# Kernel optimization log

Measured on AMD Instinct MI355X. Metric: run time of the kernel, lower is better.

Reference implementation:

```python
import jax, jax.numpy as jnp
import numpy as np

N, E, ESM, H_DIM, HEADS, LAYERS = 20000, 640000, 1280, 256, 8, 3
C = H_DIM // HEADS  # per-head channels = 32
B, M = 4096, 8


def setup_inputs() -> dict:
    key = jax.random.key(0)
    ks = jax.random.split(key, 24)
    s = lambda i, *shp: jax.random.normal(ks[i], shp, dtype=jnp.float32) * 0.02
    inp = {
        'x': jax.random.normal(ks[0], (N, ESM), dtype=jnp.float32),
        'edge_index': jax.random.randint(ks[1], (2, E), 0, N),
        'sites': jax.random.randint(ks[2], (B, M), 0, N),
        'mut_onehot': jax.random.normal(ks[3], (B, M, 20), dtype=jnp.float32),
        'mask': jnp.ones((B, M), dtype=bool),
        # params
        'in_W': s(4, ESM, H_DIM), 'in_b': jnp.zeros((H_DIM,), jnp.float32),
        'gat_W': s(5, LAYERS, H_DIM, HEADS * C),
        'att_src': s(6, LAYERS, HEADS, C), 'att_dst': s(7, LAYERS, HEADS, C),
        'gat_b': jnp.zeros((LAYERS, H_DIM), jnp.float32),
        'ln_g': jnp.ones((LAYERS, H_DIM), jnp.float32),
        'ln_b': jnp.zeros((LAYERS, H_DIM), jnp.float32),
        'me_W1': s(8, 20, H_DIM), 'me_b1': jnp.zeros((H_DIM,), jnp.float32),
        'me_W2': s(9, H_DIM, H_DIM), 'me_b2': jnp.zeros((H_DIM,), jnp.float32),
        'pool_q': jax.random.normal(ks[10], (H_DIM,), dtype=jnp.float32),
        'key_W': s(11, H_DIM, H_DIM), 'key_b': jnp.zeros((H_DIM,), jnp.float32),
        'mlp_W1': s(12, H_DIM, H_DIM // 2), 'mlp_b1': jnp.zeros((H_DIM // 2,), jnp.float32),
        'mlp_W2': s(13, H_DIM // 2, 1), 'mlp_b2': jnp.zeros((1,), jnp.float32),
    }
    return inp


def layer_norm(h, g, b, eps=1e-5):
    mu = h.mean(-1, keepdims=True)
    var = ((h - mu) ** 2).mean(-1, keepdims=True)
    return (h - mu) * jax.lax.rsqrt(var + eps) * g + b


def gat_conv(h, src, dst, W, a_src, a_dst, b):
    # PyG GATConv: linear -> per-node attn logits -> edge leaky_relu -> segment softmax over dst -> scatter-sum
    xh = (h @ W).reshape(N, HEADS, C)
    al_s = (xh * a_src).sum(-1)  # [N,H]
    al_d = (xh * a_dst).sum(-1)
    alpha = jax.nn.leaky_relu(al_s[src] + al_d[dst], negative_slope=0.2)  # [E',H]
    mx = jax.ops.segment_max(alpha, dst, num_segments=N)
    ea = jnp.exp(alpha - mx[dst])
    denom = jax.ops.segment_sum(ea, dst, num_segments=N)
    w = ea / (denom[dst] + 1e-16)
    msg = xh[src] * w[:, :, None]  # [E',H,C]
    out = jax.ops.segment_sum(msg, dst, num_segments=N)
    return out.reshape(N, HEADS * C) + b


def reference(x, edge_index, sites, mut_onehot, mask, in_W, in_b, gat_W, att_src, att_dst,
              gat_b, ln_g, ln_b, me_W1, me_b1, me_W2, me_b2, pool_q, key_W, key_b,
              mlp_W1, mlp_b1, mlp_W2, mlp_b2):
    # GATConv default add_self_loops=True
    loops = jnp.arange(N, dtype=edge_index.dtype)
    src = jnp.concatenate([edge_index[0], loops])
    dst = jnp.concatenate([edge_index[1], loops])
    # encode_graph (eval mode: dropout = identity)
    h = x @ in_W + in_b
    for i in range(LAYERS):
        h_new = gat_conv(h, src, dst, gat_W[i], att_src[i][None], att_dst[i][None], gat_b[i])
        h_new = jax.nn.elu(h_new)
        h = layer_norm(h_new + h, ln_g[i], ln_b[i])
    # predict_batch
    site_embeds = h[sites]  # [B,M,H_DIM]
    mut_embeds = jax.nn.relu(mut_onehot @ me_W1 + me_b1) @ me_W2 + me_b2
    combined = site_embeds + mut_embeds
    keys = combined @ key_W + key_b
    scores = (pool_q * keys).sum(-1) / np.sqrt(H_DIM).astype(np.float32)
    scores = jnp.where(mask, scores, -jnp.inf)
    weights = jax.nn.softmax(scores, axis=-1)[..., None]
    pooled = (weights * combined).sum(axis=1)  # [B,H_DIM]
    out = jax.nn.relu(pooled @ mlp_W1 + mlp_b1) @ mlp_W2 + mlp_b2
    return out.squeeze(-1)
```

## Files before the change

kernel.cpp:

```cpp
#include <hip/hip_runtime.h>
#include <math.h>

#define N_NODES 20000
#define N_EDGES 640000
#define E_TOT   (N_EDGES + N_NODES)
#define HD 256
#define NH 8
#define CH 32
#define NB 4096
#define NM 8

typedef short bf16x8 __attribute__((ext_vector_type(8)));
typedef float f32x4  __attribute__((ext_vector_type(4)));

__device__ __forceinline__ ushort f2bf(float f) {
  uint u = __float_as_uint(f);
  u += 0x7FFFu + ((u >> 16) & 1u);
  return (ushort)(u >> 16);
}
__device__ __forceinline__ float bf2f(ushort s) {
  return __uint_as_float(((uint)s) << 16);
}

__global__ __launch_bounds__(256) void k_wtrans(
    const float* __restrict__ W, ushort* __restrict__ WT,
    int K, int N, int strideW, int strideWT)
{
  __shared__ float tile[64][65];
  const float* Wp = W + (size_t)blockIdx.z * strideW;
  ushort* WTp = WT + (size_t)blockIdx.z * strideWT;
  int n0 = blockIdx.x * 64, k0 = blockIdx.y * 64;
  int t = threadIdx.x;
  int c = t & 63, r0 = (t >> 6) * 16;
#pragma unroll
  for (int i = 0; i < 16; ++i)
    tile[r0 + i][c] = Wp[(size_t)(k0 + r0 + i) * N + n0 + c];
  __syncthreads();
#pragma unroll
  for (int i = 0; i < 16; ++i)
    WTp[(size_t)(n0 + r0 + i) * K + k0 + c] = f2bf(tile[c][r0 + i]);
}

template<int MODE>
__global__ __launch_bounds__(256, 2) void k_gemm_mfma(
    const void* __restrict__ Ain, const ushort* __restrict__ BT,
    const float* __restrict__ bias, float* __restrict__ Cf,
    ushort* __restrict__ Cb, int M, int K)
{
  __shared__ ushort As[128 * 32];
  __shared__ ushort Bs[128 * 32];
  const int t = threadIdx.x;
  const int n0 = blockIdx.x * 128;
  const int m0 = blockIdx.y * 128;
  const int wave = t >> 6, lane = t & 63;
  const int wm = (wave & 1) * 64, wn = (wave >> 1) * 64;
  const int lm = lane & 15, quad = lane >> 4;

  f32x4 acc[4][4];
#pragma unroll
  for (int mi = 0; mi < 4; ++mi)
#pragma unroll
    for (int ni = 0; ni < 4; ++ni) acc[mi][ni] = (f32x4){0.f, 0.f, 0.f, 0.f};

  for (int k0 = 0; k0 < K; k0 += 32) {
#pragma unroll
    for (int cch = 0; cch < 2; ++cch) {
      int id = t + cch * 256;
      int row = id >> 2, j = id & 3;
      int sw = (j ^ (row & 3)) * 8;
      int ar = min(m0 + row, M - 1);
      if (MODE == 0) {
        const float* src = (const float*)Ain + (size_t)ar * K + k0 + j * 8;
        float4 u = *(const float4*)src;
        float4 v = *(const float4*)(src + 4);
        uint4 p;
        p.x = (uint)f2bf(u.x) | ((uint)f2bf(u.y) << 16);
        p.y = (uint)f2bf(u.z) | ((uint)f2bf(u.w) << 16);
        p.z = (uint)f2bf(v.x) | ((uint)f2bf(v.y) << 16);
        p.w = (uint)f2bf(v.z) | ((uint)f2bf(v.w) << 16);
        *(uint4*)&As[row * 32 + sw] = p;
      } else {
        const ushort* src = (const ushort*)Ain + (size_t)ar * K + k0 + j * 8;
        *(uint4*)&As[row * 32 + sw] = *(const uint4*)src;
      }
      const ushort* bsrc = BT + (size_t)(n0 + row) * K + k0 + j * 8;
      *(uint4*)&Bs[row * 32 + sw] = *(const uint4*)bsrc;
    }
    __syncthreads();
    bf16x8 af[4], bfr[4];
#pragma unroll
    for (int mi = 0; mi < 4; ++mi) {
      int row = wm + mi * 16 + lm;
      af[mi] = *(const bf16x8*)&As[row * 32 + ((quad ^ (row & 3)) << 3)];
    }
#pragma unroll
    for (int ni = 0; ni < 4; ++ni) {
      int row = wn + ni * 16 + lm;
      bfr[ni] = *(const bf16x8*)&Bs[row * 32 + ((quad ^ (row & 3)) << 3)];
    }
#pragma unroll
    for (int mi = 0; mi < 4; ++mi)
#pragma unroll
      for (int ni = 0; ni < 4; ++ni)
        acc[mi][ni] = __builtin_amdgcn_mfma_f32_16x16x32_bf16(af[mi], bfr[ni], acc[mi][ni], 0, 0, 0);
    __syncthreads();
  }

#pragma unroll
  for (int mi = 0; mi < 4; ++mi) {
#pragma unroll
    for (int r = 0; r < 4; ++r) {
      int row = m0 + wm + mi * 16 + quad * 4 + r;
      if (row < M) {
#pragma unroll
        for (int ni = 0; ni < 4; ++ni) {
          int col = n0 + wn + ni * 16 + lm;
          float vv = acc[mi][ni][r];
          if (MODE == 0) {
            float o = vv + bias[col];
            Cf[(size_t)row * HD + col] = o;
            Cb[(size_t)row * HD + col] = f2bf(o);
          } else {
            Cb[(size_t)row * HD + col] = f2bf(vv);
          }
        }
      }
    }
  }
}

__global__ void k_setconst(int* __restrict__ p, int n, int v) {
  int i = blockIdx.x * blockDim.x + threadIdx.x;
  if (i < n) p[i] = v;
}

__global__ void k_count(const int* __restrict__ dst, int* __restrict__ cnt) {
  int e = blockIdx.x * blockDim.x + threadIdx.x;
  if (e < N_EDGES) atomicAdd(&cnt[dst[e]], 1);
}

__global__ __launch_bounds__(1024) void k_scanA(const int* __restrict__ cnt,
                                                int* __restrict__ sc, int* __restrict__ tot) {
  __shared__ int wsum[16];
  int g = blockIdx.x * 1024 + threadIdx.x;
  int lane = threadIdx.x & 63, w = threadIdx.x >> 6;
  int v = (g < N_NODES) ? cnt[g] : 0;
#pragma unroll
  for (int off = 1; off < 64; off <<= 1) {
    int u = __shfl_up(v, off);
    if (lane >= off) v += u;
  }
  if (lane == 63) wsum[w] = v;
  __syncthreads();
  if (w == 0) {
    int s = (lane < 16) ? wsum[lane] : 0;
#pragma unroll
    for (int off = 1; off < 16; off <<= 1) {
      int u = __shfl_up(s, off);
      if (lane >= off) s += u;
    }
    if (lane < 16) wsum[lane] = s;
  }
  __syncthreads();
  if (w > 0) v += wsum[w - 1];
  if (g < N_NODES) sc[g] = v;
  if (threadIdx.x == 1023) tot[blockIdx.x] = v;
}

__global__ void k_scanB(int* __restrict__ tot) {
  int lane = threadIdx.x;
  int v = (lane < 20) ? tot[lane] : 0;
#pragma unroll
  for (int off = 1; off < 32; off <<= 1) {
    int u = __shfl_up(v, off);
    if (lane >= off) v += u;
  }
  int e = __shfl_up(v, 1);
  if (lane == 0) e = 0;
  if (lane < 20) tot[lane] = e;
}

__global__ __launch_bounds__(1024) void k_scanC(const int* __restrict__ sc,
                                                const int* __restrict__ tot,
                                                int* __restrict__ row_ptr) {
  int g = blockIdx.x * 1024 + threadIdx.x;
  if (g < N_NODES) row_ptr[g + 1] = sc[g] + tot[blockIdx.x];
  if (g == 0) row_ptr[0] = 0;
}

__global__ void k_fill(const int* __restrict__ ei, const int* __restrict__ row_ptr,
                       int* __restrict__ fill, int* __restrict__ csr) {
  int idx = blockIdx.x * blockDim.x + threadIdx.x;
  if (idx >= E_TOT) return;
  int s, d;
  if (idx < N_EDGES) { s = ei[idx]; d = ei[N_EDGES + idx]; }
  else               { s = idx - N_EDGES; d = s; }
  int p = atomicAdd(&fill[d], 1);
  csr[row_ptr[d] + p] = s;
}

__global__ void k_attn(const ushort* __restrict__ xh,
                       const float* __restrict__ att_s,
                       const float* __restrict__ att_d,
                       float* __restrict__ al_s, float* __restrict__ al_d)
{
  int idx = blockIdx.x * blockDim.x + threadIdx.x;
  if (idx >= N_NODES * NH) return;
  int hh = idx & 7;
  const ushort* row = xh + (size_t)(idx >> 3) * HD + hh * CH;
  const float4* a4  = (const float4*)(att_s + hh * CH);
  const float4* b4  = (const float4*)(att_d + hh * CH);
  float s = 0.f, d = 0.f;
#pragma unroll
  for (int q = 0; q < 8; ++q) {
    ushort4 xv = *(const ushort4*)(row + q * 4);
    float4 a = a4[q], b = b4[q];
    float v0 = bf2f(xv.x), v1 = bf2f(xv.y), v2 = bf2f(xv.z), v3 = bf2f(xv.w);
    s += v0 * a.x + v1 * a.y + v2 * a.z + v3 * a.w;
    d += v0 * b.x + v1 * b.y + v2 * b.z + v3 * b.w;
  }
  al_s[idx] = s;
  al_d[idx] = d;
}

__global__ __launch_bounds__(256) void k_aggregate(
    const ushort* __restrict__ xh, const float* __restrict__ al_s,
    const float* __restrict__ al_d, const int* __restrict__ row_ptr,
    const int* __restrict__ csr_src, const float* __restrict__ gat_b,
    const float* __restrict__ ln_g, const float* __restrict__ ln_b,
    float* __restrict__ h, ushort* __restrict__ h_bf)
{
  __shared__ float s_ea[4][64][9];
  __shared__ int   s_src[4][64];
  __shared__ int   s_deg[4];
  const int t = threadIdx.x;
  const int w = t >> 6, lane = t & 63;
  const int node = blockIdx.x * 4 + w;
  const int base = row_ptr[node];
  const int deg  = row_ptr[node + 1] - base;
  if (lane == 0) s_deg[w] = deg;
  __syncthreads();
  const int maxdeg = max(max(s_deg[0], s_deg[1]), max(s_deg[2], s_deg[3]));
  const int chunks = (maxdeg + 63) >> 6;

  float ald[8];
  {
    float4 a0 = *(const float4*)(al_d + (size_t)node * NH);
    float4 a1 = *(const float4*)(al_d + (size_t)node * NH + 4);
    ald[0] = a0.x; ald[1] = a0.y; ald[2] = a0.z; ald[3] = a0.w;
    ald[4] = a1.x; ald[5] = a1.y; ald[6] = a1.z; ald[7] = a1.w;
  }
  const int hh = lane >> 3;
  float4 acc = {0.f, 0.f, 0.f, 0.f};
  float den = 0.f;

  for (int c = 0; c < chunks; ++c) {
    const int cs = c << 6;
    int n = deg - cs; n = (n > 64) ? 64 : n;
    if (lane < n) {
      int s = csr_src[base + cs + lane];
      s_src[w][lane] = s;
      float4 b0 = *(const float4*)(al_s + (size_t)s * NH);
      float4 b1 = *(const float4*)(al_s + (size_t)s * NH + 4);
      float al[8] = {b0.x, b0.y, b0.z, b0.w, b1.x, b1.y, b1.z, b1.w};
#pragma unroll
      for (int q = 0; q < 8; ++q) {
        float a = al[q] + ald[q];
        a = fmaxf(a, 0.2f * a);
        s_ea[w][lane][q] = __expf(a);
      }
    }
    __syncthreads();
    for (int e = 0; e < n; ++e) {
      float wa = s_ea[w][e][hh];
      int s = s_src[w][e];
      den += wa;
      ushort4 xv = *(const ushort4*)(xh + (size_t)s * HD + lane * 4);
      acc.x = fmaf(wa, bf2f(xv.x), acc.x);
      acc.y = fmaf(wa, bf2f(xv.y), acc.y);
      acc.z = fmaf(wa, bf2f(xv.z), acc.z);
      acc.w = fmaf(wa, bf2f(xv.w), acc.w);
    }
    __syncthreads();
  }

  const float inv = 1.f / (den + 1e-16f);
  float4 g4 = *(const float4*)(gat_b + lane * 4);
  float4 v;
  v.x = acc.x * inv + g4.x;
  v.y = acc.y * inv + g4.y;
  v.z = acc.z * inv + g4.z;
  v.w = acc.w * inv + g4.w;
  v.x = (v.x > 0.f) ? v.x : (__expf(v.x) - 1.f);
  v.y = (v.y > 0.f) ? v.y : (__expf(v.y) - 1.f);
  v.z = (v.z > 0.f) ? v.z : (__expf(v.z) - 1.f);
  v.w = (v.w > 0.f) ? v.w : (__expf(v.w) - 1.f);
  float4 hres = *(const float4*)(h + (size_t)node * HD + lane * 4);
  v.x += hres.x; v.y += hres.y; v.z += hres.z; v.w += hres.w;

  float sum = v.x + v.y + v.z + v.w;
#pragma unroll
  for (int off = 32; off > 0; off >>= 1) sum += __shfl_xor(sum, off);
  const float mu = sum * (1.f / 256.f);
  float dx = v.x - mu, dy = v.y - mu, dz = v.z - mu, dw = v.w - mu;
  float ss = dx * dx + dy * dy + dz * dz + dw * dw;
#pragma unroll
  for (int off = 32; off > 0; off >>= 1) ss += __shfl_xor(ss, off);
  const float r = rsqrtf(ss * (1.f / 256.f) + 1e-5f);
  float4 lg = *(const float4*)(ln_g + lane * 4);
  float4 lb = *(const float4*)(ln_b + lane * 4);
  float4 o;
  o.x = dx * r * lg.x + lb.x;
  o.y = dy * r * lg.y + lb.y;
  o.z = dz * r * lg.z + lb.z;
  o.w = dw * r * lg.w + lb.w;
  *(float4*)(h + (size_t)node * HD + lane * 4) = o;
  ushort4 ob;
  ob.x = f2bf(o.x); ob.y = f2bf(o.y); ob.z = f2bf(o.z); ob.w = f2bf(o.w);
  *(ushort4*)(h_bf + (size_t)node * HD + lane * 4) = ob;
}

__global__ __launch_bounds__(256) void k_qk(const float* __restrict__ key_W,
                                            const float* __restrict__ key_b,
                                            const float* __restrict__ pool_q,
                                            float* __restrict__ qk)
{
  __shared__ float sq[HD];
  int t = threadIdx.x;
  sq[t] = pool_q[t];
  __syncthreads();
  float a = 0.f;
  for (int j = 0; j < HD; ++j) a = fmaf(key_W[(size_t)t * HD + j], sq[j], a);
  qk[t] = a;
  if (t == 0) {
    float qb = 0.f;
    for (int j = 0; j < HD; ++j) qb += sq[j] * key_b[j];
    qk[HD] = qb;
  }
}

__global__ __launch_bounds__(256, 3) void k_gemm_mut(
    const float* __restrict__ onehot, const float* __restrict__ me_W1,
    const float* __restrict__ me_b1,  const float* __restrict__ me_W2,
    const float* __restrict__ me_b2,  const float* __restrict__ h,
    const int* __restrict__ sites,    const unsigned char* __restrict__ mask8,
    const float* __restrict__ qk,     float* __restrict__ pooled)
{
  __shared__ float s_W1[20][256];
  __shared__ float s_ohT[20][64];
  __shared__ float s_b1[256], s_b2[256], s_qk[256];
  __shared__ float s_qb;
  __shared__ __align__(16) float As[8][68];
  __shared__ __align__(16) float Bs[8][260];
  __shared__ float s_scores[64];
  __shared__ int   s_site[64];
  const int t = threadIdx.x;
  const int rows0 = blockIdx.x * 64;
  const int tx = t & 31, ty = t >> 5;

  for (int i = t; i < 64 * 20; i += 256)
    s_ohT[i % 20][i / 20] = onehot[(size_t)(rows0 + i / 20) * 20 + i % 20];
  for (int i = t; i < 20 * 256; i += 256)
    s_W1[i >> 8][i & 255] = me_W1[i];
  s_b1[t] = me_b1[t];
  s_b2[t] = me_b2[t];
  s_qk[t] = qk[t];
  if (t == 0) s_qb = qk[HD];
  if (t < 64) s_site[t] = sites[rows0 + t];

  float acc[8][8];
#pragma unroll
  for (int i = 0; i < 8; ++i)
#pragma unroll
    for (int j = 0; j < 8; ++j) acc[i][j] = 0.f;

  const int r_st  = t & 63;
  const int kk_st = t >> 6;

  for (int k0 = 0; k0 < HD; k0 += 8) {
    __syncthreads();
    float ohr[20];
#pragma unroll
    for (int j = 0; j < 20; ++j) ohr[j] = s_ohT[j][r_st];
#pragma unroll
    for (int p = 0; p < 2; ++p) {
      int kk = kk_st + p * 4;
      int k  = k0 + kk;
      float v = s_b1[k];
#pragma unroll
      for (int j = 0; j < 20; ++j) v = fmaf(ohr[j], s_W1[j][k], v);
      As[kk][r_st] = fmaxf(v, 0.f);
    }
#pragma unroll
    for (int p = 0; p < 2; ++p) {
      int i = t + p * 256;
      int kk = i >> 6, c = (i & 63) * 4;
      *(float4*)&Bs[kk][c] = *(const float4*)&me_W2[(size_t)(k0 + kk) * HD + c];
    }
    __syncthreads();
#pragma unroll
    for (int k = 0; k < 8; ++k) {
      float4 a0 = *(const float4*)&As[k][ty * 8];
      float4 a1 = *(const float4*)&As[k][ty * 8 + 4];
      float4 b0 = *(const float4*)&Bs[k][tx * 4];
      float4 b1 = *(const float4*)&Bs[k][128 + tx * 4];
      float aa[8] = {a0.x, a0.y, a0.z, a0.w, a1.x, a1.y, a1.z, a1.w};
      float bb[8] = {b0.x, b0.y, b0.z, b0.w, b1.x, b1.y, b1.z, b1.w};
#pragma unroll
      for (int mi = 0; mi < 8; ++mi)
#pragma unroll
        for (int ni = 0; ni < 8; ++ni)
          acc[mi][ni] = fmaf(aa[mi], bb[ni], acc[mi][ni]);
    }
  }

  const int c0 = tx * 4, c1 = 128 + tx * 4;
#pragma unroll
  for (int mi = 0; mi < 8; ++mi) {
    int row = ty * 8 + mi;
    int s = s_site[row];
    float4 h0 = *(const float4*)(h + (size_t)s * HD + c0);
    float4 h1 = *(const float4*)(h + (size_t)s * HD + c1);
    acc[mi][0] += s_b2[c0 + 0] + h0.x;
    acc[mi][1] += s_b2[c0 + 1] + h0.y;
    acc[mi][2] += s_b2[c0 + 2] + h0.z;
    acc[mi][3] += s_b2[c0 + 3] + h0.w;
    acc[mi][4] += s_b2[c1 + 0] + h1.x;
    acc[mi][5] += s_b2[c1 + 1] + h1.y;
    acc[mi][6] += s_b2[c1 + 2] + h1.z;
    acc[mi][7] += s_b2[c1 + 3] + h1.w;
    float p = acc[mi][0] * s_qk[c0 + 0] + acc[mi][1] * s_qk[c0 + 1]
            + acc[mi][2] * s_qk[c0 + 2] + acc[mi][3] * s_qk[c0 + 3]
            + acc[mi][4] * s_qk[c1 + 0] + acc[mi][5] * s_qk[c1 + 1]
            + acc[mi][6] * s_qk[c1 + 2] + acc[mi][7] * s_qk[c1 + 3];
    p += __shfl_xor(p, 16); p += __shfl_xor(p, 8);
    p += __shfl_xor(p, 4);  p += __shfl_xor(p, 2); p += __shfl_xor(p, 1);
    if (tx == 0) {
      int grow = rows0 + row;
      bool mb;
      if (mask8[1] != 0) mb = mask8[grow] != 0;
      else               mb = ((const int*)mask8)[grow] != 0;
      s_scores[row] = mb ? (p + s_qb) * 0.0625f : -INFINITY;
    }
  }
  __syncthreads();
  float sc[8], mx = -INFINITY;
#pragma unroll
  for (int r = 0; r < 8; ++r) { sc[r] = s_scores[ty * 8 + r]; mx = fmaxf(mx, sc[r]); }
  float den = 0.f;
#pragma unroll
  for (int r = 0; r < 8; ++r) { sc[r] = __expf(sc[r] - mx); den += sc[r]; }
  float inv = 1.f / den;
  float4 o0, o1;
  o0.x = o0.y = o0.z = o0.w = o1.x = o1.y = o1.z = o1.w = 0.f;
#pragma unroll
  for (int mi = 0; mi < 8; ++mi) {
    float wgt = sc[mi] * inv;
    o0.x = fmaf(wgt, acc[mi][0], o0.x);
    o0.y = fmaf(wgt, acc[mi][1], o0.y);
    o0.z = fmaf(wgt, acc[mi][2], o0.z);
    o0.w = fmaf(wgt, acc[mi][3], o0.w);
    o1.x = fmaf(wgt, acc[mi][4], o1.x);
    o1.y = fmaf(wgt, acc[mi][5], o1.y);
    o1.z = fmaf(wgt, acc[mi][6], o1.z);
    o1.w = fmaf(wgt, acc[mi][7], o1.w);
  }
  int b = blockIdx.x * 8 + ty;
  *(float4*)(pooled + (size_t)b * HD + c0) = o0;
  *(float4*)(pooled + (size_t)b * HD + c1) = o1;
}

__global__ __launch_bounds__(128) void k_mlp(
    const float* __restrict__ pooled, const float* __restrict__ W1,
    const float* __restrict__ b1, const float* __restrict__ W2,
    const float* __restrict__ b2, float* __restrict__ out)
{
  __shared__ float s_p[16][256];
  __shared__ float s_red[16][128];
  const int t = threadIdx.x;
  const int r0 = blockIdx.x * 16;
  for (int i = t; i < 16 * 256; i += 128) {
    int r = i >> 8, cc = i & 255;
    s_p[r][cc] = pooled[(size_t)(r0 + r) * HD + cc];
  }
  __syncthreads();
  float accm[16];
#pragma unroll
  for (int r = 0; r < 16; ++r) accm[r] = 0.f;
  for (int i = 0; i < 256; ++i) {
    float w = W1[(size_t)i * 128 + t];
#pragma unroll
    for (int r = 0; r < 16; ++r) accm[r] = fmaf(s_p[r][i], w, accm[r]);
  }
  float w2 = W2[t], bb1 = b1[t];
#pragma unroll
  for (int r = 0; r < 16; ++r) s_red[r][t] = fmaxf(accm[r] + bb1, 0.f) * w2;
  __syncthreads();
  if (t < 16) {
    float s = b2[0];
    for (int j = 0; j < 128; ++j) s += s_red[t][j];
    out[r0 + t] = s;
  }
}

extern "C" void kernel_launch(void* const* d_in, const int* in_sizes, int n_in,
                              void* d_out, int out_size, void* d_ws, size_t ws_size,
                              hipStream_t stream) {
  (void)in_sizes; (void)n_in; (void)out_size; (void)ws_size;
  const float* x        = (const float*)d_in[0];
  const int*   ei       = (const int*)d_in[1];
  const int*   sites    = (const int*)d_in[2];
  const float* onehot   = (const float*)d_in[3];
  const unsigned char* mask = (const unsigned char*)d_in[4];
  const float* in_W     = (const float*)d_in[5];
  const float* in_b     = (const float*)d_in[6];
  const float* gat_W    = (const float*)d_in[7];
  const float* att_src  = (const float*)d_in[8];
  const float* att_dst  = (const float*)d_in[9];
  const float* gat_b    = (const float*)d_in[10];
  const float* ln_g     = (const float*)d_in[11];
  const float* ln_b     = (const float*)d_in[12];
  const float* me_W1    = (const float*)d_in[13];
  const float* me_b1    = (const float*)d_in[14];
  const float* me_W2    = (const float*)d_in[15];
  const float* me_b2    = (const float*)d_in[16];
  const float* pool_q   = (const float*)d_in[17];
  const float* key_W    = (const float*)d_in[18];
  const float* key_b    = (const float*)d_in[19];
  const float* mlp_W1   = (const float*)d_in[20];
  const float* mlp_b1   = (const float*)d_in[21];
  const float* mlp_W2   = (const float*)d_in[22];
  const float* mlp_b2   = (const float*)d_in[23];
  float* outp = (float*)d_out;

  char* w = (char*)d_ws;
  float*  h       = (float*)(w + 0);
  ushort* h_bf    = (ushort*)(w + 20480000);
  ushort* xh_bf   = (ushort*)(w + 30720000);
  float*  al_s    = (float*)(w + 40960000);
  float*  al_d    = (float*)(w + 41600000);
  int*    row_ptr = (int*)  (w + 42240000);
  int*    cnt     = (int*)  (w + 42320128);
  int*    csr     = (int*)  (w + 42400128);
  float*  qk      = (float*)(w + 45040128);
  float*  pooled  = (float*)(w + 45041408);
  int*    sc      = (int*)pooled;
  int*    tot     = sc + N_NODES;
  ushort* in_WT   = (ushort*)((char*)pooled + 131072);
  ushort* gat_WT  = (ushort*)((char*)pooled + 786432);

  k_wtrans<<<dim3(4, 20, 1), 256, 0, stream>>>(in_W, in_WT, 1280, HD, 0, 0);
  k_wtrans<<<dim3(4, 4, 3), 256, 0, stream>>>(gat_W, gat_WT, HD, HD, HD * HD, HD * HD);

  k_gemm_mfma<0><<<dim3(2, 157), 256, 0, stream>>>(x, in_WT, in_b, h, h_bf, N_NODES, 1280);

  k_setconst<<<(N_NODES + 255) / 256, 256, 0, stream>>>(cnt, N_NODES, 1);
  k_count<<<(N_EDGES + 255) / 256, 256, 0, stream>>>(ei + N_EDGES, cnt);
  k_scanA<<<20, 1024, 0, stream>>>(cnt, sc, tot);
  k_scanB<<<1, 64, 0, stream>>>(tot);
  k_scanC<<<20, 1024, 0, stream>>>(sc, tot, row_ptr);
  k_setconst<<<(N_NODES + 255) / 256, 256, 0, stream>>>(cnt, N_NODES, 0);
  k_fill<<<(E_TOT + 255) / 256, 256, 0, stream>>>(ei, row_ptr, cnt, csr);

  for (int l = 0; l < 3; ++l) {
    k_gemm_mfma<1><<<dim3(2, 157), 256, 0, stream>>>(h_bf, gat_WT + (size_t)l * HD * HD,
                                                     nullptr, nullptr, xh_bf, N_NODES, HD);
    k_attn<<<(N_NODES * NH + 255) / 256, 256, 0, stream>>>(xh_bf, att_src + l * NH * CH,
                                                           att_dst + l * NH * CH, al_s, al_d);
    k_aggregate<<<N_NODES / 4, 256, 0, stream>>>(xh_bf, al_s, al_d, row_ptr, csr,
                                                 gat_b + l * HD, ln_g + l * HD, ln_b + l * HD,
                                                 h, h_bf);
  }

  k_qk<<<1, 256, 0, stream>>>(key_W, key_b, pool_q, qk);
  k_gemm_mut<<<NB / 8, 256, 0, stream>>>(onehot, me_W1, me_b1, me_W2, me_b2,
                                         h, sites, mask, qk, pooled);
  k_mlp<<<NB / 16, 128, 0, stream>>>(pooled, mlp_W1, mlp_b1, mlp_W2, mlp_b2, outp);
}
```

Measured before the change: 649.5 us.

## Prefetch GEMM tiles into registers and move mutation GEMM to bf16 MFMA

The main MFMA GEMM now loads the next K-tile from global memory into registers while the current tile is computed, overlapping load latency with math. The mutation-embedding path is split into a small first-layer kernel that writes bf16 activations, and an MFMA bf16 GEMM against a transposed me_W2. That GEMM fuses the site gather, score, softmax and pooling. This replaces the fp32 FMA GEMM with tensor cores, at the cost of bf16 precision, an extra intermediate buffer and extra launches.

Result: slower. 699.7 us (+7.7%).

```diff
diff --git a/kernel.cpp b/kernel.cpp
--- a/kernel.cpp
+++ b/kernel.cpp
@@ -62,31 +62,57 @@
 #pragma unroll
     for (int ni = 0; ni < 4; ++ni) acc[mi][ni] = (f32x4){0.f, 0.f, 0.f, 0.f};
 
+  int rowc[2], jc[2], arc[2];
+#pragma unroll
+  for (int cch = 0; cch < 2; ++cch) {
+    int id = t + cch * 256;
+    rowc[cch] = id >> 2;
+    jc[cch]   = id & 3;
+    arc[cch]  = min(m0 + rowc[cch], M - 1);
+  }
+
+  float4 pa0[2], pa1[2];
+  uint4  paB[2];
+  uint4  pb[2];
+
+#define LOAD_TILE(K0)                                                          \
+  {                                                                            \
+    _Pragma("unroll")                                                          \
+    for (int cch = 0; cch < 2; ++cch) {                                        \
+      if (MODE == 0) {                                                         \
+        const float* src = (const float*)Ain + (size_t)arc[cch] * K + (K0) + jc[cch] * 8; \
+        pa0[cch] = *(const float4*)src;                                        \
+        pa1[cch] = *(const float4*)(src + 4);                                  \
+      } else {                                                                 \
+        const ushort* src = (const ushort*)Ain + (size_t)arc[cch] * K + (K0) + jc[cch] * 8; \
+        paB[cch] = *(const uint4*)src;                                         \
+      }                                                                        \
+      pb[cch] = *(const uint4*)(BT + (size_t)(n0 + rowc[cch]) * K + (K0) + jc[cch] * 8); \
+    }                                                                          \
+  }
+
+  LOAD_TILE(0);
+
   for (int k0 = 0; k0 < K; k0 += 32) {
 #pragma unroll
     for (int cch = 0; cch < 2; ++cch) {
-      int id = t + cch * 256;
-      int row = id >> 2, j = id & 3;
-      int sw = (j ^ (row & 3)) * 8;
-      int ar = min(m0 + row, M - 1);
+      int row = rowc[cch];
+      int sw = (jc[cch] ^ (row & 3)) * 8;
       if (MODE == 0) {
-        const float* src = (const float*)Ain + (size_t)ar * K + k0 + j * 8;
-        float4 u = *(const float4*)src;
-        float4 v = *(const float4*)(src + 4);
         uint4 p;
-        p.x = (uint)f2bf(u.x) | ((uint)f2bf(u.y) << 16);
-        p.y = (uint)f2bf(u.z) | ((uint)f2bf(u.w) << 16);
-        p.z = (uint)f2bf(v.x) | ((uint)f2bf(v.y) << 16);
-        p.w = (uint)f2bf(v.z) | ((uint)f2bf(v.w) << 16);
+        p.x = (uint)f2bf(pa0[cch].x) | ((uint)f2bf(pa0[cch].y) << 16);
+        p.y = (uint)f2bf(pa0[cch].z) | ((uint)f2bf(pa0[cch].w) << 16);
+        p.z = (uint)f2bf(pa1[cch].x) | ((uint)f2bf(pa1[cch].y) << 16);
+        p.w = (uint)f2bf(pa1[cch].z) | ((uint)f2bf(pa1[cch].w) << 16);
         *(uint4*)&As[row * 32 + sw] = p;
       } else {
-        const ushort* src = (const ushort*)Ain + (size_t)ar * K + k0 + j * 8;
-        *(uint4*)&As[row * 32 + sw] = *(const uint4*)src;
+        *(uint4*)&As[row * 32 + sw] = paB[cch];
       }
-      const ushort* bsrc = BT + (size_t)(n0 + row) * K + k0 + j * 8;
-      *(uint4*)&Bs[row * 32 + sw] = *(const uint4*)bsrc;
+      *(uint4*)&Bs[row * 32 + sw] = pb[cch];
     }
     __syncthreads();
+    if (k0 + 32 < K) LOAD_TILE(k0 + 32);
+
     bf16x8 af[4], bfr[4];
 #pragma unroll
     for (int mi = 0; mi < 4; ++mi) {
@@ -105,6 +131,7 @@
         acc[mi][ni] = __builtin_amdgcn_mfma_f32_16x16x32_bf16(af[mi], bfr[ni], acc[mi][ni], 0, 0, 0);
     __syncthreads();
   }
+#undef LOAD_TILE
 
 #pragma unroll
   for (int mi = 0; mi < 4; ++mi) {
@@ -339,135 +366,177 @@
   }
 }
 
-__global__ __launch_bounds__(256, 3) void k_gemm_mut(
-    const float* __restrict__ onehot, const float* __restrict__ me_W1,
-    const float* __restrict__ me_b1,  const float* __restrict__ me_W2,
-    const float* __restrict__ me_b2,  const float* __restrict__ h,
-    const int* __restrict__ sites,    const unsigned char* __restrict__ mask8,
-    const float* __restrict__ qk,     float* __restrict__ pooled)
-{
-  __shared__ float s_W1[20][256];
-  __shared__ float s_ohT[20][64];
-  __shared__ float s_b1[256], s_b2[256], s_qk[256];
-  __shared__ float s_qb;
-  __shared__ __align__(16) float As[8][68];
-  __shared__ __align__(16) float Bs[8][260];
-  __shared__ float s_scores[64];
+__global__ __launch_bounds__(256) void k_mut1(
+    const float* __restrict__ onehot, const float* __restrict__ W1,
+    const float* __restrict__ b1, ushort* __restrict__ m1)
+{
+  __shared__ float s_oh[128][20];
+  const int t = threadIdx.x;
+  const int r0 = blockIdx.x * 128;
+  float wreg[20];
+#pragma unroll
+  for (int j = 0; j < 20; ++j) wreg[j] = W1[j * HD + t];
+  const float bb = b1[t];
+  for (int i = t; i < 128 * 20; i += 256)
+    s_oh[i / 20][i % 20] = onehot[(size_t)r0 * 20 + i];
+  __syncthreads();
+  for (int r = 0; r < 128; ++r) {
+    float v = bb;
+#pragma unroll
+    for (int j = 0; j < 20; ++j) v = fmaf(s_oh[r][j], wreg[j], v);
+    m1[(size_t)(r0 + r) * HD + t] = f2bf(fmaxf(v, 0.f));
+  }
+}
+
+__global__ __launch_bounds__(256, 2) void k_gemm_mut2(
+    const ushort* __restrict__ m1, const ushort* __restrict__ W2T,
+    const float* __restrict__ me_b2, const float* __restrict__ h,
+    const int* __restrict__ sites, const unsigned char* __restrict__ mask8,
+    const float* __restrict__ qk, float* __restrict__ pooled)
+{
+  __shared__ ushort As[64 * 32];
+  __shared__ ushort Bs[256 * 32];
+  __shared__ float s_part[64][4];
+  __shared__ float s_w[64];
   __shared__ int   s_site[64];
   const int t = threadIdx.x;
   const int rows0 = blockIdx.x * 64;
-  const int tx = t & 31, ty = t >> 5;
-
-  for (int i = t; i < 64 * 20; i += 256)
-    s_ohT[i % 20][i / 20] = onehot[(size_t)(rows0 + i / 20) * 20 + i % 20];
-  for (int i = t; i < 20 * 256; i += 256)
-    s_W1[i >> 8][i & 255] = me_W1[i];
-  s_b1[t] = me_b1[t];
-  s_b2[t] = me_b2[t];
-  s_qk[t] = qk[t];
-  if (t == 0) s_qb = qk[HD];
+  const int wave = t >> 6, lane = t & 63;
+  const int wn = wave * 64;
+  const int lm = lane & 15, quad = lane >> 4;
+
   if (t < 64) s_site[t] = sites[rows0 + t];
 
-  float acc[8][8];
-#pragma unroll
-  for (int i = 0; i < 8; ++i)
-#pragma unroll
-    for (int j = 0; j < 8; ++j) acc[i][j] = 0.f;
-
-  const int r_st  = t & 63;
-  const int kk_st = t >> 6;
-
-  for (int k0 = 0; k0 < HD; k0 += 8) {
+  f32x4 acc[4][4];
+#pragma unroll
+  for (int mi = 0; mi < 4; ++mi)
+#pragma unroll
+    for (int ni = 0; ni < 4; ++ni) acc[mi][ni] = (f32x4){0.f, 0.f, 0.f, 0.f};
+
+  const int a_row = t >> 2, a_j = t & 3;
+  uint4 pa;
+  uint4 pbv[4];
+#define LOAD_MUT(K0)                                                           \
+  {                                                                            \
+    pa = *(const uint4*)(m1 + (size_t)(rows0 + a_row) * HD + (K0) + a_j * 8);  \
+    _Pragma("unroll")                                                          \
+    for (int p = 0; p < 4; ++p) {                                              \
+      int id = t + p * 256;                                                    \
+      int row = id >> 2, j = id & 3;                                           \
+      pbv[p] = *(const uint4*)(W2T + (size_t)row * HD + (K0) + j * 8);         \
+    }                                                                          \
+  }
+
+  LOAD_MUT(0);
+  for (int k0 = 0; k0 < HD; k0 += 32) {
+    {
+      int sw = (a_j ^ (a_row & 3)) * 8;
+      *(uint4*)&As[a_row * 32 + sw] = pa;
+#pragma unroll
+      for (int p = 0; p < 4; ++p) {
+        int id = t + p * 256;
+        int row = id >> 2, j = id & 3;
+        *(uint4*)&Bs[row * 32 + ((j ^ (row & 3)) * 8)] = pbv[p];
+      }
+    }
     __syncthreads();
-    float ohr[20];
-#pragma unroll
-    for (int j = 0; j < 20; ++j) ohr[j] = s_ohT[j][r_st];
-#pragma unroll
-    for (int p = 0; p < 2; ++p) {
-      int kk = kk_st + p * 4;
-      int k  = k0 + kk;
-      float v = s_b1[k];
-#pragma unroll
-      for (int j = 0; j < 20; ++j) v = fmaf(ohr[j], s_W1[j][k], v);
-      As[kk][r_st] = fmaxf(v, 0.f);
-    }
-#pragma unroll
-    for (int p = 0; p < 2; ++p) {
-      int i = t + p * 256;
-      int kk = i >> 6, c = (i & 63) * 4;
-      *(float4*)&Bs[kk][c] = *(const float4*)&me_W2[(size_t)(k0 + kk) * HD + c];
-    }
+    if (k0 + 32 < HD) LOAD_MUT(k0 + 32);
+
+    bf16x8 af[4], bfr[4];
+#pragma unroll
+    for (int mi = 0; mi < 4; ++mi) {
+      int row = mi * 16 + lm;
+      af[mi] = *(const bf16x8*)&As[row * 32 + ((quad ^ (row & 3)) << 3)];
+    }
+#pragma unroll
+    for (int ni = 0; ni < 4; ++ni) {
+      int row = wn + ni * 16 + lm;
+      bfr[ni] = *(const bf16x8*)&Bs[row * 32 + ((quad ^ (row & 3)) << 3)];
+    }
+#pragma unroll
+    for (int mi = 0; mi < 4; ++mi)
+#pragma unroll
+      for (int ni = 0; ni < 4; ++ni)
+        acc[mi][ni] = __builtin_amdgcn_mfma_f32_16x16x32_bf16(af[mi], bfr[ni], acc[mi][ni], 0, 0, 0);
     __syncthreads();
-#pragma unroll
-    for (int k = 0; k < 8; ++k) {
-      float4 a0 = *(const float4*)&As[k][ty * 8];
-      float4 a1 = *(const float4*)&As[k][ty * 8 + 4];
-      float4 b0 = *(const float4*)&Bs[k][tx * 4];
-      float4 b1 = *(const float4*)&Bs[k][128 + tx * 4];
-      float aa[8] = {a0.x, a0.y, a0.z, a0.w, a1.x, a1.y, a1.z, a1.w};
-      float bb[8] = {b0.x, b0.y, b0.z, b0.w, b1.x, b1.y, b1.z, b1.w};
-#pragma unroll
-      for (int mi = 0; mi < 8; ++mi)
-#pragma unroll
-        for (int ni = 0; ni < 8; ++ni)
-          acc[mi][ni] = fmaf(aa[mi], bb[ni], acc[mi][ni]);
-    }
-  }
-
-  const int c0 = tx * 4, c1 = 128 + tx * 4;
-#pragma unroll
-  for (int mi = 0; mi < 8; ++mi) {
-    int row = ty * 8 + mi;
-    int s = s_site[row];
-    float4 h0 = *(const float4*)(h + (size_t)s * HD + c0);
-    float4 h1 = *(const float4*)(h + (size_t)s * HD + c1);
-    acc[mi][0] += s_b2[c0 + 0] + h0.x;
-    acc[mi][1] += s_b2[c0 + 1] + h0.y;
-    acc[mi][2] += s_b2[c0 + 2] + h0.z;
-    acc[mi][3] += s_b2[c0 + 3] + h0.w;
-    acc[mi][4] += s_b2[c1 + 0] + h1.x;
-    acc[mi][5] += s_b2[c1 + 1] + h1.y;
-    acc[mi][6] += s_b2[c1 + 2] + h1.z;
-    acc[mi][7] += s_b2[c1 + 3] + h1.w;
-    float p = acc[mi][0] * s_qk[c0 + 0] + acc[mi][1] * s_qk[c0 + 1]
-            + acc[mi][2] * s_qk[c0 + 2] + acc[mi][3] * s_qk[c0 + 3]
-            + acc[mi][4] * s_qk[c1 + 0] + acc[mi][5] * s_qk[c1 + 1]
-            + acc[mi][6] * s_qk[c1 + 2] + acc[mi][7] * s_qk[c1 + 3];
-    p += __shfl_xor(p, 16); p += __shfl_xor(p, 8);
-    p += __shfl_xor(p, 4);  p += __shfl_xor(p, 2); p += __shfl_xor(p, 1);
-    if (tx == 0) {
-      int grow = rows0 + row;
-      bool mb;
-      if (mask8[1] != 0) mb = mask8[grow] != 0;
-      else               mb = ((const int*)mask8)[grow] != 0;
-      s_scores[row] = mb ? (p + s_qb) * 0.0625f : -INFINITY;
-    }
-  }
-  __syncthreads();
-  float sc[8], mx = -INFINITY;
-#pragma unroll
-  for (int r = 0; r < 8; ++r) { sc[r] = s_scores[ty * 8 + r]; mx = fmaxf(mx, sc[r]); }
-  float den = 0.f;
-#pragma unroll
-  for (int r = 0; r < 8; ++r) { sc[r] = __expf(sc[r] - mx); den += sc[r]; }
-  float inv = 1.f / den;
-  float4 o0, o1;
-  o0.x = o0.y = o0.z = o0.w = o1.x = o1.y = o1.z = o1.w = 0.f;
-#pragma unroll
-  for (int mi = 0; mi < 8; ++mi) {
-    float wgt = sc[mi] * inv;
-    o0.x = fmaf(wgt, acc[mi][0], o0.x);
-    o0.y = fmaf(wgt, acc[mi][1], o0.y);
-    o0.z = fmaf(wgt, acc[mi][2], o0.z);
-    o0.w = fmaf(wgt, acc[mi][3], o0.w);
-    o1.x = fmaf(wgt, acc[mi][4], o1.x);
-    o1.y = fmaf(wgt, acc[mi][5], o1.y);
-    o1.z = fmaf(wgt, acc[mi][6], o1.z);
-    o1.w = fmaf(wgt, acc[mi][7], o1.w);
-  }
-  int b = blockIdx.x * 8 + ty;
-  *(float4*)(pooled + (size_t)b * HD + c0) = o0;
-  *(float4*)(pooled + (size_t)b * HD + c1) = o1;
+  }
+#undef LOAD_MUT
+
+  float pscore[4][4];
+#pragma unroll
+  for (int mi = 0; mi < 4; ++mi)
+#pragma unroll
+    for (int r = 0; r < 4; ++r) pscore[mi][r] = 0.f;
+
+#pragma unroll
+  for (int ni = 0; ni < 4; ++ni) {
+    int col = wn + ni * 16 + lm;
+    float qkc = qk[col];
+    float b2c = me_b2[col];
+#pragma unroll
+    for (int mi = 0; mi < 4; ++mi) {
+#pragma unroll
+      for (int r = 0; r < 4; ++r) {
+        int row = mi * 16 + quad * 4 + r;
+        float c = acc[mi][ni][r] + b2c + h[(size_t)s_site[row] * HD + col];
+        acc[mi][ni][r] = c;
+        pscore[mi][r] = fmaf(c, qkc, pscore[mi][r]);
+      }
+    }
+  }
+#pragma unroll
+  for (int mi = 0; mi < 4; ++mi)
+#pragma unroll
+    for (int r = 0; r < 4; ++r) {
+      float p = pscore[mi][r];
+      p += __shfl_xor(p, 8); p += __shfl_xor(p, 4);
+      p += __shfl_xor(p, 2); p += __shfl_xor(p, 1);
+      pscore[mi][r] = p;
+    }
+  if (lm == 0) {
+#pragma unroll
+    for (int mi = 0; mi < 4; ++mi)
+#pragma unroll
+      for (int r = 0; r < 4; ++r)
+        s_part[mi * 16 + quad * 4 + r][wave] = pscore[mi][r];
+  }
+  __syncthreads();
+  if (t < 64) {
+    float s = s_part[t][0] + s_part[t][1] + s_part[t][2] + s_part[t][3];
+    s = (s + qk[HD]) * 0.0625f;
+    int grow = rows0 + t;
+    bool mb;
+    if (mask8[1] != 0) mb = mask8[grow] != 0;
+    else               mb = ((const int*)mask8)[grow] != 0;
+    s_w[t] = mb ? s : -INFINITY;
+  }
+  __syncthreads();
+  if (t < 8) {
+    float e[NM], mx = -INFINITY, den = 0.f;
+#pragma unroll
+    for (int m = 0; m < NM; ++m) mx = fmaxf(mx, s_w[t * NM + m]);
+#pragma unroll
+    for (int m = 0; m < NM; ++m) { e[m] = __expf(s_w[t * NM + m] - mx); den += e[m]; }
+    float inv = 1.f / den;
+#pragma unroll
+    for (int m = 0; m < NM; ++m) s_w[t * NM + m] = e[m] * inv;
+  }
+  __syncthreads();
+#pragma unroll
+  for (int ni = 0; ni < 4; ++ni) {
+    int col = wn + ni * 16 + lm;
+#pragma unroll
+    for (int mi = 0; mi < 4; ++mi) {
+      float pp = 0.f;
+#pragma unroll
+      for (int r = 0; r < 4; ++r)
+        pp = fmaf(s_w[mi * 16 + quad * 4 + r], acc[mi][ni][r], pp);
+      pp += __shfl_xor(pp, 16);
+      int b = mi * 2 + (quad >> 1);
+      if ((quad & 1) == 0)
+        pooled[(size_t)(blockIdx.x * 8 + b) * HD + col] = pp;
+    }
+  }
 }
 
 __global__ __launch_bounds__(128) void k_mlp(
@@ -548,6 +617,8 @@
   int*    tot     = sc + N_NODES;
   ushort* in_WT   = (ushort*)((char*)pooled + 131072);
   ushort* gat_WT  = (ushort*)((char*)pooled + 786432);
+  ushort* m1      = (ushort*)(w + 20480000);
+  ushort* me_W2T  = (ushort*)(w + 40960000);
 
   k_wtrans<<<dim3(4, 20, 1), 256, 0, stream>>>(in_W, in_WT, 1280, HD, 0, 0);
   k_wtrans<<<dim3(4, 4, 3), 256, 0, stream>>>(gat_W, gat_WT, HD, HD, HD * HD, HD * HD);
@@ -572,8 +643,9 @@
                                                  h, h_bf);
   }
 
+  k_wtrans<<<dim3(4, 4, 1), 256, 0, stream>>>(me_W2, me_W2T, HD, HD, 0, 0);
+  k_mut1<<<NB * NM / 128, 256, 0, stream>>>(onehot, me_W1, me_b1, m1);
   k_qk<<<1, 256, 0, stream>>>(key_W, key_b, pool_q, qk);
-  k_gemm_mut<<<NB / 8, 256, 0, stream>>>(onehot, me_W1, me_b1, me_W2, me_b2,
-                                         h, sites, mask, qk, pooled);
+  k_gemm_mut2<<<NB * NM / 64, 256, 0, stream>>>(m1, me_W2T, me_b2, h, sites, mask, qk, pooled);
   k_mlp<<<NB / 16, 128, 0, stream>>>(pooled, mlp_W1, mlp_b1, mlp_W2, mlp_b2, outp);
 }
```
